# Kernel optimization log

Hardware: AMD Instinct MI355X
Metric: run time of the kernel (lower is better)

## Reference

```python
import jax, jax.numpy as jnp
import numpy as np

H = 1024   # hidden_size == embedding_dim (forced by the 2*hidden concat/view)
A = 256    # attention_hidden_size
V = 50257  # vocab_size
L = 2      # num_layers
T = 512    # decoder length
S = 512    # encoder length


def setup_inputs() -> dict:
    key = jax.random.key(0)
    ks = jax.random.split(key, 24)
    f = lambda i, shape: (0.02 * jax.random.normal(ks[i], shape)).astype(jnp.float32)
    return {
        "decoder_input": jax.random.randint(ks[0], (T,), 0, V),
        "encoder_outputs": jax.random.normal(ks[1], (S, H), dtype=jnp.float32),
        "emb": f(2, (V, H)),
        # attn (context attention over encoder outputs): Linear(2H->A) split into x/ctx parts, v: Linear(A->1)
        "Wa_x": f(3, (A, H)), "Wa_c": f(4, (A, H)), "ba": f(5, (A,)), "va": f(6, (A,)), "vab": f(7, ()),
        # GRU cells (torch GRUCell param layout: [r; z; n] stacked, 3H rows)
        "Wih0": f(8, (3 * H, 2 * H)), "bih0": f(9, (3 * H,)), "Whh0": f(10, (3 * H, H)), "bhh0": f(11, (3 * H,)),
        "Wih1": f(12, (3 * H, H)), "bih1": f(13, (3 * H,)), "Whh1": f(14, (3 * H, H)), "bhh1": f(15, (3 * H,)),
        # per-layer hidden self-attentions (no context)
        "Wh": f(16, (L, A, H)), "bh": f(17, (L, A)), "vh": f(18, (L, A)), "vhb": f(19, (L,)),
        # output head
        "Wf1": f(20, (32, H)), "bf1": f(21, (32,)), "Wf2": f(22, (V, 32)), "bf2": f(23, (V,)),
    }


def _attn(x, Wx, b, v, vb, ctx=None, Wc=None):
    # additive attention: e_t = v . tanh(W_x x_t + W_c c + b); weighted sum over axis 0
    pre = x @ Wx.T + b                      # [T, A]
    if ctx is not None:
        pre = pre + ctx @ Wc.T              # broadcast [A]
    e = jnp.tanh(pre) @ v + vb              # [T]
    return jax.nn.softmax(e) @ x            # [D]


def _gru(x, h, Wih, bih, Whh, bhh):
    gi = Wih @ x + bih
    gh = Whh @ h + bhh
    ir, iz, inn = jnp.split(gi, 3)
    hr, hz, hn = jnp.split(gh, 3)
    r = jax.nn.sigmoid(ir + hr)
    z = jax.nn.sigmoid(iz + hz)
    n = jnp.tanh(inn + r * hn)
    return (1.0 - z) * n + z * h


def reference(decoder_input, encoder_outputs, emb, Wa_x, Wa_c, ba, va, vab,
              Wih0, bih0, Whh0, bhh0, Wih1, bih1, Whh1, bhh1,
              Wh, bh, vh, vhb, Wf1, bf1, Wf2, bf2):
    tok_embs = emb[decoder_input]           # [T, H]

    def step(carry, tok):
        h0, h1 = carry
        a = _attn(encoder_outputs, Wa_x, ba, va, vab, ctx=h0, Wc=Wa_c)  # [H]
        x = jnp.concatenate([a, tok])                                   # [2H]
        nh0 = _gru(x, h0, Wih0, bih0, Whh0, bhh0)
        nh1 = _gru(nh0, h1, Wih1, bih1, Whh1, bhh1)
        # hidden attention i combines new_h_s[i:]
        h0n = _attn(jnp.stack([nh0, nh1]), Wh[0], bh[0], vh[0], vhb[0])
        h1n = _attn(nh1[None, :], Wh[1], bh[1], vh[1], vhb[1])           # softmax over 1 elem == nh1
        fc1 = jax.nn.relu(Wf1 @ h1n + bf1)                               # dropout = eval-mode identity
        out = jax.nn.softmax(Wf2 @ fc1 + bf2)                            # softmax over vocab (dim 0)
        return (h0n, h1n), out

    h0 = jnp.zeros((Whh0.shape[1],), jnp.float32)
    _, outs = jax.lax.scan(step, (h0, h0), tok_embs)
    return outs  # [T, V]
```

## Files before the change

### kernel.cpp

```cpp
#include <hip/hip_runtime.h>
#include <cstdint>
#include <cstddef>

#define T_LEN 512
#define S_LEN 512
#define HID   1024
#define AD    256
#define VOC   50257
#define G3    3072
#define NWG   256
#define NT    512
#define NPART (197*4)

#define WS_GENC   0
#define WS_GITOK  (WS_GENC + G3*S_LEN)
#define WS_EX     (WS_GITOK + T_LEN*G3)
#define WS_H1     (WS_EX + S_LEN*AD)
#define WS_FC1    (WS_H1 + T_LEN*HID)
#define WS_NH0    (WS_FC1 + T_LEN*32)
#define WS_NH1    (WS_NH0 + HID)
#define WS_WB     (WS_NH1 + HID)
#define WS_U0     (WS_WB + S_LEN)
#define WS_U1     (WS_U0 + AD)
#define WS_E0P    (WS_U1 + AD)
#define WS_E1P    (WS_E0P + 256)
#define WS_BARX   (WS_E1P + 256)
#define WS_ROWP   (WS_BARX + 384)
#define WS_INV    (WS_ROWP + T_LEN*NPART)
#define WS_END    (WS_INV + T_LEN)

__device__ inline float wred64(float v) {
  v += __shfl_xor(v, 32, 64); v += __shfl_xor(v, 16, 64); v += __shfl_xor(v, 8, 64);
  v += __shfl_xor(v, 4, 64);  v += __shfl_xor(v, 2, 64);  v += __shfl_xor(v, 1, 64);
  return v;
}

__device__ inline float fast_sigmoid(float x) { return 1.f / (1.f + __expf(-x)); }
__device__ inline float fast_tanh(float x) {
  float e = __expf(2.f * x);
  return 1.f - 2.f / (e + 1.f);
}

__device__ inline float ldw(const float* p) {
  return __uint_as_float(__hip_atomic_load((const unsigned int*)p,
                                           __ATOMIC_RELAXED, __HIP_MEMORY_SCOPE_AGENT));
}
__device__ inline void stw(float* p, float v) {
  __hip_atomic_store((unsigned int*)p, __float_as_uint(v),
                     __ATOMIC_RELAXED, __HIP_MEMORY_SCOPE_AGENT);
}
__device__ inline unsigned ldu(const unsigned* p) {
  return __hip_atomic_load(p, __ATOMIC_RELAXED, __HIP_MEMORY_SCOPE_AGENT);
}
__device__ inline void stu(unsigned* p, unsigned v) {
  __hip_atomic_store(p, v, __ATOMIC_RELAXED, __HIP_MEMORY_SCOPE_AGENT);
}

__device__ inline void gbar(unsigned* slot, unsigned* gen, unsigned b) {
  __syncthreads();
  if (threadIdx.x == 0) stu(slot + blockIdx.x, b);
  if (blockIdx.x == 0) {
    if (threadIdx.x < NWG) {
      while (ldu(slot + threadIdx.x) < b) __builtin_amdgcn_s_sleep(1);
    }
    __syncthreads();
    if (threadIdx.x == 0) stu(gen, b);
  } else {
    if (threadIdx.x == 0) {
      while (ldu(gen) < b) __builtin_amdgcn_s_sleep(1);
    }
    __syncthreads();
  }
}

__device__ inline float qdot4(const float4& a0, const float4& a1, const float4& a2, const float4& a3,
                              const float4& x0, const float4& x1, const float4& x2, const float4& x3) {
  float a = 0.f;
  a = fmaf(a0.x, x0.x, a); a = fmaf(a0.y, x0.y, a); a = fmaf(a0.z, x0.z, a); a = fmaf(a0.w, x0.w, a);
  a = fmaf(a1.x, x1.x, a); a = fmaf(a1.y, x1.y, a); a = fmaf(a1.z, x1.z, a); a = fmaf(a1.w, x1.w, a);
  a = fmaf(a2.x, x2.x, a); a = fmaf(a2.y, x2.y, a); a = fmaf(a2.z, x2.z, a); a = fmaf(a2.w, x2.w, a);
  a = fmaf(a3.x, x3.x, a); a = fmaf(a3.y, x3.y, a); a = fmaf(a3.z, x3.z, a); a = fmaf(a3.w, x3.w, a);
  return a;
}
__device__ inline float qdot2(const float4& a0, const float4& a1,
                              const float4& x0, const float4& x1) {
  float a = 0.f;
  a = fmaf(a0.x, x0.x, a); a = fmaf(a0.y, x0.y, a); a = fmaf(a0.z, x0.z, a); a = fmaf(a0.w, x0.w, a);
  a = fmaf(a1.x, x1.x, a); a = fmaf(a1.y, x1.y, a); a = fmaf(a1.z, x1.z, a); a = fmaf(a1.w, x1.w, a);
  return a;
}

__global__ void k_init(float* ws) {
  const int tid = threadIdx.x;
  for (int i = tid; i < HID; i += 256) { ws[WS_NH0 + i] = 0.f; ws[WS_NH1 + i] = 0.f; }
  if (tid < AD) { ws[WS_U0 + tid] = 0.f; ws[WS_U1 + tid] = 0.f; }
  ws[WS_E0P + tid] = 0.f;
  ws[WS_E1P + tid] = 0.f;
  for (int i = tid; i < 384; i += 256) ((unsigned*)(ws + WS_BARX))[i] = 0u;
}

__global__ __launch_bounds__(256) void k_gemm(
    const float* __restrict__ A, int lda, const int* __restrict__ gidx,
    const float* __restrict__ B, int ldb, int kofs,
    const float* __restrict__ bias, float* __restrict__ C, int ldc,
    int M, int N, int act)
{
  __shared__ float As[64][33];
  __shared__ float Bs[64][33];
  const int bm = blockIdx.y * 64, bn = blockIdx.x * 64;
  const int tx = threadIdx.x & 15, ty = threadIdx.x >> 4;
  float acc[4][4] = {};
  const int lin = threadIdx.x * 8;
  const int lr = lin >> 5;
  const int lc = lin & 31;
  for (int k0 = 0; k0 < 1024; k0 += 32) {
    {
      const int gm = bm + lr;
      float4 v0 = {0,0,0,0}, v1 = {0,0,0,0};
      if (gm < M) {
        const int row = gidx ? gidx[gm] : gm;
        const float* p = A + (size_t)row * lda + k0 + lc;
        v0 = *(const float4*)p; v1 = *(const float4*)(p + 4);
      }
      As[lr][lc+0]=v0.x; As[lr][lc+1]=v0.y; As[lr][lc+2]=v0.z; As[lr][lc+3]=v0.w;
      As[lr][lc+4]=v1.x; As[lr][lc+5]=v1.y; As[lr][lc+6]=v1.z; As[lr][lc+7]=v1.w;
    }
    {
      const int gn = bn + lr;
      float4 v0 = {0,0,0,0}, v1 = {0,0,0,0};
      if (gn < N) {
        const float* p = B + (size_t)gn * ldb + kofs + k0 + lc;
        v0 = *(const float4*)p; v1 = *(const float4*)(p + 4);
      }
      Bs[lr][lc+0]=v0.x; Bs[lr][lc+1]=v0.y; Bs[lr][lc+2]=v0.z; Bs[lr][lc+3]=v0.w;
      Bs[lr][lc+4]=v1.x; Bs[lr][lc+5]=v1.y; Bs[lr][lc+6]=v1.z; Bs[lr][lc+7]=v1.w;
    }
    __syncthreads();
    #pragma unroll
    for (int kk = 0; kk < 32; ++kk) {
      float a0 = As[ty*4+0][kk], a1 = As[ty*4+1][kk], a2 = As[ty*4+2][kk], a3 = As[ty*4+3][kk];
      float b0 = Bs[tx*4+0][kk], b1 = Bs[tx*4+1][kk], b2 = Bs[tx*4+2][kk], b3 = Bs[tx*4+3][kk];
      acc[0][0]=fmaf(a0,b0,acc[0][0]); acc[0][1]=fmaf(a0,b1,acc[0][1]); acc[0][2]=fmaf(a0,b2,acc[0][2]); acc[0][3]=fmaf(a0,b3,acc[0][3]);
      acc[1][0]=fmaf(a1,b0,acc[1][0]); acc[1][1]=fmaf(a1,b1,acc[1][1]); acc[1][2]=fmaf(a1,b2,acc[1][2]); acc[1][3]=fmaf(a1,b3,acc[1][3]);
      acc[2][0]=fmaf(a2,b0,acc[2][0]); acc[2][1]=fmaf(a2,b1,acc[2][1]); acc[2][2]=fmaf(a2,b2,acc[2][2]); acc[2][3]=fmaf(a2,b3,acc[2][3]);
      acc[3][0]=fmaf(a3,b0,acc[3][0]); acc[3][1]=fmaf(a3,b1,acc[3][1]); acc[3][2]=fmaf(a3,b2,acc[3][2]); acc[3][3]=fmaf(a3,b3,acc[3][3]);
    }
    __syncthreads();
  }
  #pragma unroll
  for (int i = 0; i < 4; ++i)
    #pragma unroll
    for (int j = 0; j < 4; ++j) {
      const int m = bm + ty*4 + i, n = bn + tx*4 + j;
      if (m < M && n < N) {
        float v = acc[i][j] + (bias ? bias[n] : 0.f);
        if (act == 1) v = fmaxf(v, 0.f);
        C[(size_t)m * ldc + n] = v;
      }
    }
}

__global__ __launch_bounds__(NT) void k_recur(
    float* __restrict__ ws,
    const float* __restrict__ Whh0, const float* __restrict__ bhh0,
    const float* __restrict__ Wih1, const float* __restrict__ bih1,
    const float* __restrict__ Whh1, const float* __restrict__ bhh1,
    const float* __restrict__ Wh,   const float* __restrict__ bh,
    const float* __restrict__ vh,   const float* __restrict__ vhb,
    const float* __restrict__ va,   const float* __restrict__ vab,
    const float* __restrict__ Wac)
{
  const float* Genc  = ws + WS_GENC;
  const float* gitok = ws + WS_GITOK;
  const float* Ex    = ws + WS_EX;
  float* H1    = ws + WS_H1;
  float* nh0g  = ws + WS_NH0;
  float* nh1g  = ws + WS_NH1;
  float* wbufg = ws + WS_WB;
  float* u0g   = ws + WS_U0;
  float* u1g   = ws + WS_U1;
  float* e0pg  = ws + WS_E0P;
  float* e1pg  = ws + WS_E1P;
  unsigned* slot = (unsigned*)(ws + WS_BARX);
  unsigned* gen  = slot + NWG;

  const int wg = blockIdx.x, tid = threadIdx.x;
  const int lane = tid & 63, wv = tid >> 6;

  __shared__ float xv[HID];
  __shared__ float wl[S_LEN];
  __shared__ float cb[AD];
  __shared__ float sgit[12], sgh0[12], gh1l[12], sb0[12], sbh1[12], sacc[12];
  __shared__ float sred[8], sal[2], ssc[1];

  float4 wreg[28];
  if (wv < 6) {
    #pragma unroll
    for (int r = 0; r < 2; ++r) {
      const int lr = 2 * wv + r;
      const int g = (lr >> 2) * HID + wg * 4 + (lr & 3);
      const float4* p0 = (const float4*)(Whh0 + (size_t)g * HID);
      const float4* p1 = (const float4*)(Wih1 + (size_t)g * HID);
      const float4* p2 = (const float4*)(Whh1 + (size_t)g * HID);
      const float4* pg = (const float4*)(Genc + (size_t)g * S_LEN);
      #pragma unroll
      for (int p = 0; p < 4; ++p) {
        wreg[r*4+p]      = p0[p*64 + lane];
        wreg[8 + r*4+p]  = p1[p*64 + lane];
        wreg[16 + r*4+p] = p2[p*64 + lane];
      }
      #pragma unroll
      for (int p = 0; p < 2; ++p) wreg[24 + r*2+p] = pg[p*64 + lane];
    }
  } else {
    const float* Wrow = (wv == 6) ? (Wh + (size_t)wg * HID) : (Wac + (size_t)wg * HID);
    const float4* p0 = (const float4*)Wrow;
    #pragma unroll
    for (int p = 0; p < 4; ++p) wreg[p] = p0[p*64 + lane];
    const int s = 2 * wg + (wv - 6);
    wreg[4] = ((const float4*)(Ex + (size_t)s * AD))[lane];
    wreg[5] = ((const float4*)va)[lane];
  }

  float i1r = 0.f, i1z = 0.f, i1n = 0.f;
  if (tid < 4) {
    const int j = wg * 4 + tid;
    i1r = bih1[j]; i1z = bih1[HID + j]; i1n = bih1[2 * HID + j];
  }
  if (tid < 12) {
    const int g = (tid >> 2) * HID + wg * 4 + (tid & 3);
    sb0[tid] = bhh0[g];
    const float bb = bhh1[g];
    sbh1[tid] = bb;
    gh1l[tid] = bb;
  }
  const float vhW = vh[wg], bhW = bh[wg];
  const float vabv = vab[0], vhb0 = vhb[0];
  unsigned b = 0;
  __syncthreads();

  const float4* XV4 = (const float4*)xv;
  const float4* WL4 = (const float4*)wl;
  const float4* CB4 = (const float4*)cb;

  #pragma unroll 1
  for (int t = 0; t < T_LEN; ++t) {
    {
      const float a0 = ldw(nh0g + tid), a1 = ldw(nh0g + 512 + tid);
      const float b0 = ldw(nh1g + tid), b1 = ldw(nh1g + 512 + tid);
      float uu0 = 0.f, uu1 = 0.f;
      if (tid < AD) { uu0 = ldw(u0g + tid); uu1 = ldw(u1g + tid); }
      float ep = (tid < 256) ? ldw(e0pg + tid) : ldw(e1pg + tid - 256);
      if (tid < 12)
        sgit[tid] = gitok[(size_t)t * G3 + (tid >> 2) * HID + wg * 4 + (tid & 3)];
      ep = wred64(ep);
      if (lane == 0) sred[wv] = ep;
      __syncthreads();
      if (tid == 0) {
        const float e0 = sred[0] + sred[1] + sred[2] + sred[3] + vhb0;
        const float e1 = sred[4] + sred[5] + sred[6] + sred[7] + vhb0;
        const float ea = __expf(e0), eb = __expf(e1);
        const float s = ea + eb;
        sal[0] = ea / s; sal[1] = eb / s;
      }
      __syncthreads();
      const float al0 = sal[0], al1 = sal[1];
      xv[tid]       = al0 * a0 + al1 * b0;
      xv[tid + 512] = al0 * a1 + al1 * b1;
      if (tid < AD) cb[tid] = al0 * uu0 + al1 * uu1;
      __syncthreads();
      if (wv < 6) {
        const float4 x0 = XV4[lane], x1 = XV4[64+lane], x2 = XV4[128+lane], x3 = XV4[192+lane];
        float accA = qdot4(wreg[0], wreg[1], wreg[2], wreg[3], x0, x1, x2, x3);
        float accB = qdot4(wreg[4], wreg[5], wreg[6], wreg[7], x0, x1, x2, x3);
        accA = wred64(accA); accB = wred64(accB);
        if (lane == 0) {
          sgh0[2*wv]     = accA + sb0[2*wv];
          sgh0[2*wv + 1] = accB + sb0[2*wv + 1];
        }
      } else {
        const float4 e4 = wreg[4], v4 = wreg[5], c4 = CB4[lane];
        const float s0 = fast_tanh(e4.x + c4.x);
        const float s1 = fast_tanh(e4.y + c4.y);
        const float s2 = fast_tanh(e4.z + c4.z);
        const float s3 = fast_tanh(e4.w + c4.w);
        float acc = v4.x*s0 + v4.y*s1 + v4.z*s2 + v4.w*s3;
        acc = wred64(acc);
        if (lane == 0) stw(wbufg + 2*wg + (wv - 6), __expf(acc + vabv));
      }
    }
    gbar(slot, gen, ++b);

    {
      const float wval = ldw(wbufg + tid);
      wl[tid] = wval;
      const float ps = wred64(wval);
      if (lane == 0) sred[wv] = ps;
      __syncthreads();
      if (tid == 0) {
        float s = 0.f;
        #pragma unroll
        for (int i = 0; i < 8; ++i) s += sred[i];
        ssc[0] = 1.f / s;
      }
      if (wv < 6) {
        const float4 w0 = WL4[lane], w1 = WL4[64 + lane];
        float accA = qdot2(wreg[24], wreg[25], w0, w1);
        float accB = qdot2(wreg[26], wreg[27], w0, w1);
        accA = wred64(accA); accB = wred64(accB);
        if (lane == 0) { sacc[2*wv] = accA; sacc[2*wv + 1] = accB; }
      }
      __syncthreads();
      if (tid < 4) {
        const float inv = ssc[0];
        const float d0 = sacc[tid]     * inv + sgit[tid];
        const float d1 = sacc[4 + tid] * inv + sgit[4 + tid];
        const float d2 = sacc[8 + tid] * inv + sgit[8 + tid];
        const float rg = fast_sigmoid(d0 + sgh0[tid]);
        const float zg = fast_sigmoid(d1 + sgh0[4 + tid]);
        const float ng = fast_tanh(d2 + rg * sgh0[8 + tid]);
        const float h0j = xv[wg * 4 + tid];
        stw(nh0g + wg * 4 + tid, (1.f - zg) * ng + zg * h0j);
      }
    }
    gbar(slot, gen, ++b);

    {
      const float x0 = ldw(nh0g + tid), x1 = ldw(nh0g + 512 + tid);
      const float oldn = (tid < 4) ? ldw(nh1g + wg * 4 + tid) : 0.f;
      xv[tid] = x0; xv[tid + 512] = x1;
      __syncthreads();
      const float4 y0 = XV4[lane], y1 = XV4[64+lane], y2 = XV4[128+lane], y3 = XV4[192+lane];
      if (wv < 6) {
        float accA = qdot4(wreg[8],  wreg[9],  wreg[10], wreg[11], y0, y1, y2, y3);
        float accB = qdot4(wreg[12], wreg[13], wreg[14], wreg[15], y0, y1, y2, y3);
        accA = wred64(accA); accB = wred64(accB);
        if (lane == 0) { sacc[2*wv] = accA; sacc[2*wv + 1] = accB; }
      } else {
        float acc = qdot4(wreg[0], wreg[1], wreg[2], wreg[3], y0, y1, y2, y3);
        acc = wred64(acc);
        if (lane == 0) {
          if (wv == 6) stw(e0pg + wg, vhW * fast_tanh(acc + bhW));
          else         stw(u0g + wg, acc);
        }
      }
      __syncthreads();
      if (tid < 4) {
        const float gr = sacc[tid]     + i1r;
        const float gz = sacc[4 + tid] + i1z;
        const float gn = sacc[8 + tid] + i1n;
        const float rg = fast_sigmoid(gr + gh1l[tid]);
        const float zg = fast_sigmoid(gz + gh1l[4 + tid]);
        const float ng = fast_tanh(gn + rg * gh1l[8 + tid]);
        const float nv = (1.f - zg) * ng + zg * oldn;
        stw(nh1g + wg * 4 + tid, nv);
        H1[(size_t)t * HID + wg * 4 + tid] = nv;
      }
    }
    gbar(slot, gen, ++b);

    {
      const float x0 = ldw(nh1g + tid), x1 = ldw(nh1g + 512 + tid);
      xv[tid] = x0; xv[tid + 512] = x1;
      __syncthreads();
      const float4 y0 = XV4[lane], y1 = XV4[64+lane], y2 = XV4[128+lane], y3 = XV4[192+lane];
      if (wv < 6) {
        float accA = qdot4(wreg[16], wreg[17], wreg[18], wreg[19], y0, y1, y2, y3);
        float accB = qdot4(wreg[20], wreg[21], wreg[22], wreg[23], y0, y1, y2, y3);
        accA = wred64(accA); accB = wred64(accB);
        if (lane == 0) {
          gh1l[2*wv]     = accA + sbh1[2*wv];
          gh1l[2*wv + 1] = accB + sbh1[2*wv + 1];
        }
      } else {
        float acc = qdot4(wreg[0], wreg[1], wreg[2], wreg[3], y0, y1, y2, y3);
        acc = wred64(acc);
        if (lane == 0) {
          if (wv == 6) stw(e1pg + wg, vhW * fast_tanh(acc + bhW));
          else         stw(u1g + wg, acc);
        }
      }
    }
    gbar(slot, gen, ++b);
  }
}

__global__ __launch_bounds__(256) void k_head(
    const float* __restrict__ FC1, const float* __restrict__ Wf2,
    const float* __restrict__ bf2, float* __restrict__ out, float* __restrict__ rowp)
{
  __shared__ float fcb[256 * 32];
  const int v = blockIdx.x * 256 + threadIdx.x;
  const bool ok = v < VOC;
  float wf[32];
  float bb = 0.f;
  if (ok) {
    const float4* W4 = (const float4*)(Wf2 + (size_t)v * 32);
    #pragma unroll
    for (int q = 0; q < 8; ++q) ((float4*)wf)[q] = W4[q];
    bb = bf2[v];
  }
  const int wv = threadIdx.x >> 6;
  #pragma unroll 1
  for (int half = 0; half < 2; ++half) {
    __syncthreads();
    for (int i = threadIdx.x; i < 256 * 32 / 4; i += 256)
      ((float4*)fcb)[i] = ((const float4*)(FC1 + half * 256 * 32))[i];
    __syncthreads();
    #pragma unroll 1
    for (int tt = 0; tt < 256; ++tt) {
      const int t = half * 256 + tt;
      const float4* f4 = (const float4*)(fcb + tt * 32);
      float acc = bb;
      #pragma unroll
      for (int q = 0; q < 8; ++q) {
        float4 f = f4[q];
        acc = fmaf(wf[4*q+0], f.x, acc);
        acc = fmaf(wf[4*q+1], f.y, acc);
        acc = fmaf(wf[4*q+2], f.z, acc);
        acc = fmaf(wf[4*q+3], f.w, acc);
      }
      const float w = ok ? __expf(acc) : 0.f;
      if (ok) out[(size_t)t * VOC + v] = w;
      float r = wred64(w);
      if ((threadIdx.x & 63) == 0)
        rowp[(size_t)t * NPART + (size_t)blockIdx.x * 4 + wv] = r;
    }
  }
}

__global__ __launch_bounds__(256) void k_rowsum(const float* __restrict__ rowp, float* __restrict__ inv) {
  const int t = blockIdx.x;
  float acc = 0.f;
  for (int i = threadIdx.x; i < NPART; i += 256) acc += rowp[(size_t)t * NPART + i];
  acc = wred64(acc);
  __shared__ float sr[4];
  if ((threadIdx.x & 63) == 0) sr[threadIdx.x >> 6] = acc;
  __syncthreads();
  if (threadIdx.x == 0) inv[t] = 1.f / (sr[0] + sr[1] + sr[2] + sr[3]);
}

__global__ __launch_bounds__(256) void k_scale(float* __restrict__ out, const float* __restrict__ inv) {
  const int t = blockIdx.y;
  const float s = inv[t];
  const size_t base = (size_t)t * VOC;
  const int v0 = blockIdx.x * 2048 + threadIdx.x;
  #pragma unroll
  for (int k = 0; k < 8; ++k) {
    const int v = v0 + k * 256;
    if (v < VOC) out[base + v] *= s;
  }
}

extern "C" void kernel_launch(void* const* d_in, const int* in_sizes, int n_in,
                              void* d_out, int out_size, void* d_ws, size_t ws_size,
                              hipStream_t stream) {
  const int*   dec  = (const int*)  d_in[0];
  const float* enc  = (const float*)d_in[1];
  const float* emb  = (const float*)d_in[2];
  const float* Wax  = (const float*)d_in[3];
  const float* Wac  = (const float*)d_in[4];
  const float* ba   = (const float*)d_in[5];
  const float* va   = (const float*)d_in[6];
  const float* vab  = (const float*)d_in[7];
  const float* Wih0 = (const float*)d_in[8];
  const float* bih0 = (const float*)d_in[9];
  const float* Whh0 = (const float*)d_in[10];
  const float* bhh0 = (const float*)d_in[11];
  const float* Wih1 = (const float*)d_in[12];
  const float* bih1 = (const float*)d_in[13];
  const float* Whh1 = (const float*)d_in[14];
  const float* bhh1 = (const float*)d_in[15];
  const float* Wh   = (const float*)d_in[16];
  const float* bh   = (const float*)d_in[17];
  const float* vh   = (const float*)d_in[18];
  const float* vhb  = (const float*)d_in[19];
  const float* Wf1  = (const float*)d_in[20];
  const float* bf1  = (const float*)d_in[21];
  const float* Wf2  = (const float*)d_in[22];
  const float* bf2  = (const float*)d_in[23];
  float* out = (float*)d_out;
  float* ws  = (float*)d_ws;

  k_init<<<1, 256, 0, stream>>>(ws);

  k_gemm<<<dim3(8, 48), 256, 0, stream>>>(Wih0, 2048, nullptr, enc, 1024, 0,
                                          nullptr, ws + WS_GENC, 512, G3, S_LEN, 0);
  k_gemm<<<dim3(48, 8), 256, 0, stream>>>(emb, 1024, dec, Wih0, 2048, 1024,
                                          bih0, ws + WS_GITOK, G3, T_LEN, G3, 0);
  k_gemm<<<dim3(4, 8), 256, 0, stream>>>(enc, 1024, nullptr, Wax, 1024, 0,
                                         ba, ws + WS_EX, AD, S_LEN, AD, 0);

  k_recur<<<NWG, NT, 0, stream>>>(ws, Whh0, bhh0, Wih1, bih1, Whh1, bhh1,
                                  Wh, bh, vh, vhb, va, vab, Wac);

  k_gemm<<<dim3(1, 8), 256, 0, stream>>>(ws + WS_H1, 1024, nullptr, Wf1, 1024, 0,
                                         bf1, ws + WS_FC1, 32, T_LEN, 32, 1);

  k_head<<<197, 256, 0, stream>>>(ws + WS_FC1, Wf2, bf2, out, ws + WS_ROWP);
  k_rowsum<<<512, 256, 0, stream>>>(ws + WS_ROWP, ws + WS_INV);
  k_scale<<<dim3(25, 512), 256, 0, stream>>>(out, ws + WS_INV);
}
```

Before: 5.518 ms.

## Replace grid barriers with tagged per-value flags and double-buffered exchange

The persistent recurrent kernel no longer runs four centralized grid barriers per timestep. Each exchanged value is now stored as a 64-bit word that packs the float with a timestep tag, double-buffered by step parity. Consumers spin until the exact values they need carry the expected tag, so workgroups sync point-to-point. A few block-level syncs and a serial thread-0 softmax are also folded into redundant per-thread computation. The change aims to remove barrier latency from the serial critical path, at the cost of many more polling atomic loads and more memory-ordering subtlety.

```diff
diff --git a/kernel.cpp b/kernel.cpp
--- a/kernel.cpp
+++ b/kernel.cpp
@@ -12,65 +12,67 @@
 #define NT    512
 #define NPART (197*4)
 
+typedef unsigned long long u64;
+
 #define WS_GENC   0
 #define WS_GITOK  (WS_GENC + G3*S_LEN)
 #define WS_EX     (WS_GITOK + T_LEN*G3)
 #define WS_H1     (WS_EX + S_LEN*AD)
 #define WS_FC1    (WS_H1 + T_LEN*HID)
-#define WS_NH0    (WS_FC1 + T_LEN*32)
-#define WS_NH1    (WS_NH0 + HID)
-#define WS_WB     (WS_NH1 + HID)
-#define WS_U0     (WS_WB + S_LEN)
-#define WS_U1     (WS_U0 + AD)
-#define WS_E0P    (WS_U1 + AD)
-#define WS_E1P    (WS_E0P + 256)
-#define WS_BARX   (WS_E1P + 256)
-#define WS_ROWP   (WS_BARX + 384)
+#define WS_ROWP   (WS_FC1 + T_LEN*32)
 #define WS_INV    (WS_ROWP + T_LEN*NPART)
-#define WS_END    (WS_INV + T_LEN)
+#define WS_TAGF   (((WS_INV + T_LEN) + 3) & ~3)
+
+#define SP 2
+#define TG_NH0 0
+#define TG_NH1 (TG_NH0 + 2*1024*SP)
+#define TG_W   (TG_NH1 + 2*1024*SP)
+#define TG_U0  (TG_W   + 2*512*SP)
+#define TG_U1  (TG_U0  + 2*256*SP)
+#define TG_E0  (TG_U1  + 2*256*SP)
+#define TG_E1  (TG_E0  + 2*256*SP)
+#define TG_TOT (TG_E1  + 2*256*SP)
 
 __device__ inline float wred64(float v) {
   v += __shfl_xor(v, 32, 64); v += __shfl_xor(v, 16, 64); v += __shfl_xor(v, 8, 64);
   v += __shfl_xor(v, 4, 64);  v += __shfl_xor(v, 2, 64);  v += __shfl_xor(v, 1, 64);
   return v;
 }
-
 __device__ inline float fast_sigmoid(float x) { return 1.f / (1.f + __expf(-x)); }
 __device__ inline float fast_tanh(float x) {
   float e = __expf(2.f * x);
   return 1.f - 2.f / (e + 1.f);
 }
 
-__device__ inline float ldw(const float* p) {
-  return __uint_as_float(__hip_atomic_load((const unsigned int*)p,
-                                           __ATOMIC_RELAXED, __HIP_MEMORY_SCOPE_AGENT));
-}
-__device__ inline void stw(float* p, float v) {
-  __hip_atomic_store((unsigned int*)p, __float_as_uint(v),
+__device__ inline u64 ald(const u64* p) {
+  return __hip_atomic_load(p, __ATOMIC_RELAXED, __HIP_MEMORY_SCOPE_AGENT);
+}
+__device__ inline void stq(u64* p, float v, unsigned tag) {
+  __hip_atomic_store(p, ((u64)tag << 32) | (u64)__float_as_uint(v),
                      __ATOMIC_RELAXED, __HIP_MEMORY_SCOPE_AGENT);
 }
-__device__ inline unsigned ldu(const unsigned* p) {
-  return __hip_atomic_load(p, __ATOMIC_RELAXED, __HIP_MEMORY_SCOPE_AGENT);
-}
-__device__ inline void stu(unsigned* p, unsigned v) {
-  __hip_atomic_store(p, v, __ATOMIC_RELAXED, __HIP_MEMORY_SCOPE_AGENT);
-}
-
-__device__ inline void gbar(unsigned* slot, unsigned* gen, unsigned b) {
-  __syncthreads();
-  if (threadIdx.x == 0) stu(slot + blockIdx.x, b);
-  if (blockIdx.x == 0) {
-    if (threadIdx.x < NWG) {
-      while (ldu(slot + threadIdx.x) < b) __builtin_amdgcn_s_sleep(1);
-    }
-    __syncthreads();
-    if (threadIdx.x == 0) stu(gen, b);
-  } else {
-    if (threadIdx.x == 0) {
-      while (ldu(gen) < b) __builtin_amdgcn_s_sleep(1);
-    }
-    __syncthreads();
-  }
+__device__ inline float poll1(const u64* p, unsigned tag) {
+  u64 x = ald(p);
+  while ((unsigned)(x >> 32) != tag) { __builtin_amdgcn_s_sleep(1); x = ald(p); }
+  return __uint_as_float((unsigned)x);
+}
+__device__ inline void poll2(const u64* p0, const u64* p1, unsigned tag, float& r0, float& r1) {
+  u64 x0 = ald(p0), x1 = ald(p1);
+  while (((unsigned)(x0 >> 32) != tag) | ((unsigned)(x1 >> 32) != tag)) {
+    __builtin_amdgcn_s_sleep(1); x0 = ald(p0); x1 = ald(p1);
+  }
+  r0 = __uint_as_float((unsigned)x0); r1 = __uint_as_float((unsigned)x1);
+}
+__device__ inline void poll4(const u64* p0, const u64* p1, const u64* p2, const u64* p3,
+                             unsigned tag, float& r0, float& r1, float& r2, float& r3) {
+  u64 x0 = ald(p0), x1 = ald(p1), x2 = ald(p2), x3 = ald(p3);
+  while (((unsigned)(x0 >> 32) != tag) | ((unsigned)(x1 >> 32) != tag) |
+         ((unsigned)(x2 >> 32) != tag) | ((unsigned)(x3 >> 32) != tag)) {
+    __builtin_amdgcn_s_sleep(1);
+    x0 = ald(p0); x1 = ald(p1); x2 = ald(p2); x3 = ald(p3);
+  }
+  r0 = __uint_as_float((unsigned)x0); r1 = __uint_as_float((unsigned)x1);
+  r2 = __uint_as_float((unsigned)x2); r3 = __uint_as_float((unsigned)x3);
 }
 
 __device__ inline float qdot4(const float4& a0, const float4& a1, const float4& a2, const float4& a3,
@@ -91,12 +93,9 @@
 }
 
 __global__ void k_init(float* ws) {
-  const int tid = threadIdx.x;
-  for (int i = tid; i < HID; i += 256) { ws[WS_NH0 + i] = 0.f; ws[WS_NH1 + i] = 0.f; }
-  if (tid < AD) { ws[WS_U0 + tid] = 0.f; ws[WS_U1 + tid] = 0.f; }
-  ws[WS_E0P + tid] = 0.f;
-  ws[WS_E1P + tid] = 0.f;
-  for (int i = tid; i < 384; i += 256) ((unsigned*)(ws + WS_BARX))[i] = 0u;
+  u64* TG = (u64*)(ws + WS_TAGF);
+  const int i = blockIdx.x * 256 + threadIdx.x;
+  if (i < TG_TOT) TG[i] = 0ull;
 }
 
 __global__ __launch_bounds__(256) void k_gemm(
@@ -173,16 +172,15 @@
   const float* Genc  = ws + WS_GENC;
   const float* gitok = ws + WS_GITOK;
   const float* Ex    = ws + WS_EX;
-  float* H1    = ws + WS_H1;
-  float* nh0g  = ws + WS_NH0;
-  float* nh1g  = ws + WS_NH1;
-  float* wbufg = ws + WS_WB;
-  float* u0g   = ws + WS_U0;
-  float* u1g   = ws + WS_U1;
-  float* e0pg  = ws + WS_E0P;
-  float* e1pg  = ws + WS_E1P;
-  unsigned* slot = (unsigned*)(ws + WS_BARX);
-  unsigned* gen  = slot + NWG;
+  float* H1 = ws + WS_H1;
+  u64* TG   = (u64*)(ws + WS_TAGF);
+  u64* tNH0 = TG + TG_NH0;
+  u64* tNH1 = TG + TG_NH1;
+  u64* tW   = TG + TG_W;
+  u64* tU0  = TG + TG_U0;
+  u64* tU1  = TG + TG_U1;
+  u64* tE0  = TG + TG_E0;
+  u64* tE1  = TG + TG_E1;
 
   const int wg = blockIdx.x, tid = threadIdx.x;
   const int lane = tid & 63, wv = tid >> 6;
@@ -190,8 +188,8 @@
   __shared__ float xv[HID];
   __shared__ float wl[S_LEN];
   __shared__ float cb[AD];
-  __shared__ float sgit[12], sgh0[12], gh1l[12], sb0[12], sbh1[12], sacc[12];
-  __shared__ float sred[8], sal[2], ssc[1];
+  __shared__ float sgh0[12], gh1l[12], sb0[12], sbh1[12], sacc[12];
+  __shared__ float sred[8];
 
   float4 wreg[28];
   if (wv < 6) {
@@ -236,7 +234,6 @@
   }
   const float vhW = vh[wg], bhW = bh[wg];
   const float vabv = vab[0], vhb0 = vhb[0];
-  unsigned b = 0;
   __syncthreads();
 
   const float4* XV4 = (const float4*)xv;
@@ -245,63 +242,71 @@
 
   #pragma unroll 1
   for (int t = 0; t < T_LEN; ++t) {
+    const int c = t & 1, pc = c ^ 1;
+    const unsigned tg = (unsigned)(t + 1);
+    const unsigned tp = (unsigned)t;
+
     {
-      const float a0 = ldw(nh0g + tid), a1 = ldw(nh0g + 512 + tid);
-      const float b0 = ldw(nh1g + tid), b1 = ldw(nh1g + 512 + tid);
-      float uu0 = 0.f, uu1 = 0.f;
-      if (tid < AD) { uu0 = ldw(u0g + tid); uu1 = ldw(u1g + tid); }
-      float ep = (tid < 256) ? ldw(e0pg + tid) : ldw(e1pg + tid - 256);
-      if (tid < 12)
-        sgit[tid] = gitok[(size_t)t * G3 + (tid >> 2) * HID + wg * 4 + (tid & 3)];
+      float a0, a1, b0, b1;
+      poll4(tNH0 + (size_t)(pc*1024 + tid)*SP, tNH0 + (size_t)(pc*1024 + 512 + tid)*SP,
+            tNH1 + (size_t)(pc*1024 + tid)*SP, tNH1 + (size_t)(pc*1024 + 512 + tid)*SP,
+            tp, a0, a1, b0, b1);
+      float ep, uu0 = 0.f, uu1 = 0.f;
+      if (tid < 256) {
+        ep = poll1(tE0 + (size_t)(pc*256 + tid)*SP, tp);
+        poll2(tU0 + (size_t)(pc*256 + tid)*SP, tU1 + (size_t)(pc*256 + tid)*SP, tp, uu0, uu1);
+      } else {
+        ep = poll1(tE1 + (size_t)(pc*256 + tid - 256)*SP, tp);
+      }
       ep = wred64(ep);
       if (lane == 0) sred[wv] = ep;
       __syncthreads();
-      if (tid == 0) {
-        const float e0 = sred[0] + sred[1] + sred[2] + sred[3] + vhb0;
-        const float e1 = sred[4] + sred[5] + sred[6] + sred[7] + vhb0;
-        const float ea = __expf(e0), eb = __expf(e1);
-        const float s = ea + eb;
-        sal[0] = ea / s; sal[1] = eb / s;
-      }
-      __syncthreads();
-      const float al0 = sal[0], al1 = sal[1];
+      const float e0s = sred[0] + sred[1] + sred[2] + sred[3] + vhb0;
+      const float e1s = sred[4] + sred[5] + sred[6] + sred[7] + vhb0;
+      const float ea = __expf(e0s), eb = __expf(e1s);
+      const float rs = 1.f / (ea + eb);
+      const float al0 = ea * rs, al1 = eb * rs;
       xv[tid]       = al0 * a0 + al1 * b0;
       xv[tid + 512] = al0 * a1 + al1 * b1;
-      if (tid < AD) cb[tid] = al0 * uu0 + al1 * uu1;
-      __syncthreads();
-      if (wv < 6) {
-        const float4 x0 = XV4[lane], x1 = XV4[64+lane], x2 = XV4[128+lane], x3 = XV4[192+lane];
-        float accA = qdot4(wreg[0], wreg[1], wreg[2], wreg[3], x0, x1, x2, x3);
-        float accB = qdot4(wreg[4], wreg[5], wreg[6], wreg[7], x0, x1, x2, x3);
-        accA = wred64(accA); accB = wred64(accB);
-        if (lane == 0) {
-          sgh0[2*wv]     = accA + sb0[2*wv];
-          sgh0[2*wv + 1] = accB + sb0[2*wv + 1];
-        }
-      } else {
-        const float4 e4 = wreg[4], v4 = wreg[5], c4 = CB4[lane];
-        const float s0 = fast_tanh(e4.x + c4.x);
-        const float s1 = fast_tanh(e4.y + c4.y);
-        const float s2 = fast_tanh(e4.z + c4.z);
-        const float s3 = fast_tanh(e4.w + c4.w);
-        float acc = v4.x*s0 + v4.y*s1 + v4.z*s2 + v4.w*s3;
-        acc = wred64(acc);
-        if (lane == 0) stw(wbufg + 2*wg + (wv - 6), __expf(acc + vabv));
-      }
-    }
-    gbar(slot, gen, ++b);
+      if (tid < 256) cb[tid] = al0 * uu0 + al1 * uu1;
+      __syncthreads();
+    }
+    float h0j = 0.f;
+    if (tid < 4) h0j = xv[wg * 4 + tid];
+    if (wv < 6) {
+      const float4 x0 = XV4[lane], x1 = XV4[64+lane], x2 = XV4[128+lane], x3 = XV4[192+lane];
+      float accA = qdot4(wreg[0], wreg[1], wreg[2], wreg[3], x0, x1, x2, x3);
+      float accB = qdot4(wreg[4], wreg[5], wreg[6], wreg[7], x0, x1, x2, x3);
+      accA = wred64(accA); accB = wred64(accB);
+      if (lane == 0) {
+        sgh0[2*wv]     = accA + sb0[2*wv];
+        sgh0[2*wv + 1] = accB + sb0[2*wv + 1];
+      }
+    } else {
+      const float4 e4 = wreg[4], v4 = wreg[5], c4 = CB4[lane];
+      float acc = v4.x * fast_tanh(e4.x + c4.x) + v4.y * fast_tanh(e4.y + c4.y)
+                + v4.z * fast_tanh(e4.z + c4.z) + v4.w * fast_tanh(e4.w + c4.w);
+      acc = wred64(acc);
+      if (lane == 0)
+        stq(tW + (size_t)(c*512 + 2*wg + (wv - 6))*SP, __expf(acc + vabv), tg);
+    }
 
     {
-      const float wval = ldw(wbufg + tid);
+      float g0 = 0.f, g1 = 0.f, g2 = 0.f;
+      if (tid < 4) {
+        const float* gp = gitok + (size_t)t * G3 + wg * 4 + tid;
+        g0 = gp[0]; g1 = gp[HID]; g2 = gp[2 * HID];
+      }
+      const float wval = poll1(tW + (size_t)(c*512 + tid)*SP, tg);
       wl[tid] = wval;
-      const float ps = wred64(wval);
-      if (lane == 0) sred[wv] = ps;
-      __syncthreads();
-      if (tid == 0) {
+      __syncthreads();
+      float inv = 0.f;
+      if (wv == 0) {
         float s = 0.f;
         #pragma unroll
-        for (int i = 0; i < 8; ++i) s += sred[i];
-        ssc[0] = 1.f / s;
+        for (int k = 0; k < 8; ++k) s += wl[lane + 64*k];
+        s = wred64(s);
+        inv = 1.f / s;
       }
       if (wv < 6) {
         const float4 w0 = WL4[lane], w1 = WL4[64 + lane];
@@ -312,22 +317,21 @@
       }
       __syncthreads();
       if (tid < 4) {
-        const float inv = ssc[0];
-        const float d0 = sacc[tid]     * inv + sgit[tid];
-        const float d1 = sacc[4 + tid] * inv + sgit[4 + tid];
-        const float d2 = sacc[8 + tid] * inv + sgit[8 + tid];
+        const float d0 = sacc[tid]     * inv + g0;
+        const float d1 = sacc[4 + tid] * inv + g1;
+        const float d2 = sacc[8 + tid] * inv + g2;
         const float rg = fast_sigmoid(d0 + sgh0[tid]);
         const float zg = fast_sigmoid(d1 + sgh0[4 + tid]);
         const float ng = fast_tanh(d2 + rg * sgh0[8 + tid]);
-        const float h0j = xv[wg * 4 + tid];
-        stw(nh0g + wg * 4 + tid, (1.f - zg) * ng + zg * h0j);
-      }
-    }
-    gbar(slot, gen, ++b);
+        stq(tNH0 + (size_t)(c*1024 + wg*4 + tid)*SP, (1.f - zg) * ng + zg * h0j, tg);
+      }
+    }
 
     {
-      const float x0 = ldw(nh0g + tid), x1 = ldw(nh0g + 512 + tid);
-      const float oldn = (tid < 4) ? ldw(nh1g + wg * 4 + tid) : 0.f;
+      float oldn = 0.f;
+      if (tid < 4) oldn = poll1(tNH1 + (size_t)(pc*1024 + wg*4 + tid)*SP, tp);
+      float x0, x1;
+      poll2(tNH0 + (size_t)(c*1024 + tid)*SP, tNH0 + (size_t)(c*1024 + 512 + tid)*SP, tg, x0, x1);
       xv[tid] = x0; xv[tid + 512] = x1;
       __syncthreads();
       const float4 y0 = XV4[lane], y1 = XV4[64+lane], y2 = XV4[128+lane], y3 = XV4[192+lane];
@@ -340,8 +344,8 @@
         float acc = qdot4(wreg[0], wreg[1], wreg[2], wreg[3], y0, y1, y2, y3);
         acc = wred64(acc);
         if (lane == 0) {
-          if (wv == 6) stw(e0pg + wg, vhW * fast_tanh(acc + bhW));
-          else         stw(u0g + wg, acc);
+          if (wv == 6) stq(tE0 + (size_t)(c*256 + wg)*SP, vhW * fast_tanh(acc + bhW), tg);
+          else         stq(tU0 + (size_t)(c*256 + wg)*SP, acc, tg);
         }
       }
       __syncthreads();
@@ -353,14 +357,14 @@
         const float zg = fast_sigmoid(gz + gh1l[4 + tid]);
         const float ng = fast_tanh(gn + rg * gh1l[8 + tid]);
         const float nv = (1.f - zg) * ng + zg * oldn;
-        stw(nh1g + wg * 4 + tid, nv);
+        stq(tNH1 + (size_t)(c*1024 + wg*4 + tid)*SP, nv, tg);
         H1[(size_t)t * HID + wg * 4 + tid] = nv;
       }
     }
-    gbar(slot, gen, ++b);
 
     {
-      const float x0 = ldw(nh1g + tid), x1 = ldw(nh1g + 512 + tid);
+      float x0, x1;
+      poll2(tNH1 + (size_t)(c*1024 + tid)*SP, tNH1 + (size_t)(c*1024 + 512 + tid)*SP, tg, x0, x1);
       xv[tid] = x0; xv[tid + 512] = x1;
       __syncthreads();
       const float4 y0 = XV4[lane], y1 = XV4[64+lane], y2 = XV4[128+lane], y3 = XV4[192+lane];
@@ -376,12 +380,11 @@
         float acc = qdot4(wreg[0], wreg[1], wreg[2], wreg[3], y0, y1, y2, y3);
         acc = wred64(acc);
         if (lane == 0) {
-          if (wv == 6) stw(e1pg + wg, vhW * fast_tanh(acc + bhW));
-          else         stw(u1g + wg, acc);
+          if (wv == 6) stq(tE1 + (size_t)(c*256 + wg)*SP, vhW * fast_tanh(acc + bhW), tg);
+          else         stq(tU1 + (size_t)(c*256 + wg)*SP, acc, tg);
         }
       }
     }
-    gbar(slot, gen, ++b);
   }
 }
 
@@ -482,7 +485,7 @@
   float* out = (float*)d_out;
   float* ws  = (float*)d_ws;
 
-  k_init<<<1, 256, 0, stream>>>(ws);
+  k_init<<<56, 256, 0, stream>>>(ws);
 
   k_gemm<<<dim3(8, 48), 256, 0, stream>>>(Wih0, 2048, nullptr, enc, 1024, 0,
                                           nullptr, ws + WS_GENC, 512, G3, S_LEN, 0);
```

Result: no change. 5.575 ms (+1.0%).

## Use two-level grid barrier and carry recurrent state in registers across steps

Applied to the files above, without the earlier changes.

Replaces the flat grid barrier, where one workgroup polled all 256 slots, with a two-level barrier. Eight leader workgroups each gather 32 slots, synchronise among themselves, then release per-group generation flags, and arrival stores now use release ordering. The recurrent loop also keeps the previous nh0/nh1 values, the e0p/u0 partials and the old layer-1 hidden value in registers, and prefetches the next step's gitok slice during the last phase. This removes redundant global reloads at the start of each step. The barrier area now overlaps the start of the rowp workspace region, which is only safe if the head kernel runs after the recurrence.

```diff
diff --git a/kernel.cpp b/kernel.cpp
--- a/kernel.cpp
+++ b/kernel.cpp
@@ -25,7 +25,7 @@
 #define WS_E0P    (WS_U1 + AD)
 #define WS_E1P    (WS_E0P + 256)
 #define WS_BARX   (WS_E1P + 256)
-#define WS_ROWP   (WS_BARX + 384)
+#define WS_ROWP   (WS_BARX + 128)
 #define WS_INV    (WS_ROWP + T_LEN*NPART)
 #define WS_END    (WS_INV + T_LEN)
 
@@ -52,42 +52,37 @@
 __device__ inline unsigned ldu(const unsigned* p) {
   return __hip_atomic_load(p, __ATOMIC_RELAXED, __HIP_MEMORY_SCOPE_AGENT);
 }
-__device__ inline void stu(unsigned* p, unsigned v) {
-  __hip_atomic_store(p, v, __ATOMIC_RELAXED, __HIP_MEMORY_SCOPE_AGENT);
-}
-
-__device__ inline void gbar(unsigned* slot, unsigned* gen, unsigned b) {
+__device__ inline void stu_rel(unsigned* p, unsigned v) {
+  __hip_atomic_store(p, v, __ATOMIC_RELEASE, __HIP_MEMORY_SCOPE_AGENT);
+}
+
+__device__ inline void gbar(unsigned* bar, int wg, unsigned b) {
+  unsigned* slots = bar;
+  unsigned* xa    = bar + 256;
+  unsigned* geng  = bar + 384;
+  const int g = wg & 7;
   __syncthreads();
-  if (threadIdx.x == 0) stu(slot + blockIdx.x, b);
-  if (blockIdx.x == 0) {
-    if (threadIdx.x < NWG) {
-      while (ldu(slot + threadIdx.x) < b) __builtin_amdgcn_s_sleep(1);
+  if (threadIdx.x == 0) stu_rel(slots + g * 32 + (wg >> 3), b);
+  if (wg < 8) {
+    if (threadIdx.x < 32) {
+      const unsigned* p = slots + wg * 32 + threadIdx.x;
+      while (ldu(p) < b) __builtin_amdgcn_s_sleep(1);
     }
     __syncthreads();
-    if (threadIdx.x == 0) stu(gen, b);
+    if (threadIdx.x == 0) stu_rel(xa + wg * 16, b);
+    if (threadIdx.x < 8) {
+      const unsigned* p = xa + threadIdx.x * 16;
+      while (ldu(p) < b) __builtin_amdgcn_s_sleep(1);
+    }
+    __syncthreads();
+    if (threadIdx.x == 0) stu_rel(geng + wg * 16, b);
   } else {
     if (threadIdx.x == 0) {
-      while (ldu(gen) < b) __builtin_amdgcn_s_sleep(1);
-    }
-    __syncthreads();
-  }
-}
-
-__device__ inline float qdot4(const float4& a0, const float4& a1, const float4& a2, const float4& a3,
-                              const float4& x0, const float4& x1, const float4& x2, const float4& x3) {
-  float a = 0.f;
-  a = fmaf(a0.x, x0.x, a); a = fmaf(a0.y, x0.y, a); a = fmaf(a0.z, x0.z, a); a = fmaf(a0.w, x0.w, a);
-  a = fmaf(a1.x, x1.x, a); a = fmaf(a1.y, x1.y, a); a = fmaf(a1.z, x1.z, a); a = fmaf(a1.w, x1.w, a);
-  a = fmaf(a2.x, x2.x, a); a = fmaf(a2.y, x2.y, a); a = fmaf(a2.z, x2.z, a); a = fmaf(a2.w, x2.w, a);
-  a = fmaf(a3.x, x3.x, a); a = fmaf(a3.y, x3.y, a); a = fmaf(a3.z, x3.z, a); a = fmaf(a3.w, x3.w, a);
-  return a;
-}
-__device__ inline float qdot2(const float4& a0, const float4& a1,
-                              const float4& x0, const float4& x1) {
-  float a = 0.f;
-  a = fmaf(a0.x, x0.x, a); a = fmaf(a0.y, x0.y, a); a = fmaf(a0.z, x0.z, a); a = fmaf(a0.w, x0.w, a);
-  a = fmaf(a1.x, x1.x, a); a = fmaf(a1.y, x1.y, a); a = fmaf(a1.z, x1.z, a); a = fmaf(a1.w, x1.w, a);
-  return a;
+      const unsigned* p = geng + g * 16;
+      while (ldu(p) < b) __builtin_amdgcn_s_sleep(1);
+    }
+  }
+  __syncthreads();
 }
 
 __global__ void k_init(float* ws) {
@@ -96,7 +91,7 @@
   if (tid < AD) { ws[WS_U0 + tid] = 0.f; ws[WS_U1 + tid] = 0.f; }
   ws[WS_E0P + tid] = 0.f;
   ws[WS_E1P + tid] = 0.f;
-  for (int i = tid; i < 384; i += 256) ((unsigned*)(ws + WS_BARX))[i] = 0u;
+  for (int i = tid; i < 512; i += 256) ((unsigned*)(ws + WS_BARX))[i] = 0u;
 }
 
 __global__ __launch_bounds__(256) void k_gemm(
@@ -160,6 +155,23 @@
     }
 }
 
+__device__ inline float qdot4(const float4& a0, const float4& a1, const float4& a2, const float4& a3,
+                              const float4& x0, const float4& x1, const float4& x2, const float4& x3) {
+  float a = 0.f;
+  a = fmaf(a0.x, x0.x, a); a = fmaf(a0.y, x0.y, a); a = fmaf(a0.z, x0.z, a); a = fmaf(a0.w, x0.w, a);
+  a = fmaf(a1.x, x1.x, a); a = fmaf(a1.y, x1.y, a); a = fmaf(a1.z, x1.z, a); a = fmaf(a1.w, x1.w, a);
+  a = fmaf(a2.x, x2.x, a); a = fmaf(a2.y, x2.y, a); a = fmaf(a2.z, x2.z, a); a = fmaf(a2.w, x2.w, a);
+  a = fmaf(a3.x, x3.x, a); a = fmaf(a3.y, x3.y, a); a = fmaf(a3.z, x3.z, a); a = fmaf(a3.w, x3.w, a);
+  return a;
+}
+__device__ inline float qdot2(const float4& a0, const float4& a1,
+                              const float4& x0, const float4& x1) {
+  float a = 0.f;
+  a = fmaf(a0.x, x0.x, a); a = fmaf(a0.y, x0.y, a); a = fmaf(a0.z, x0.z, a); a = fmaf(a0.w, x0.w, a);
+  a = fmaf(a1.x, x1.x, a); a = fmaf(a1.y, x1.y, a); a = fmaf(a1.z, x1.z, a); a = fmaf(a1.w, x1.w, a);
+  return a;
+}
+
 __global__ __launch_bounds__(NT) void k_recur(
     float* __restrict__ ws,
     const float* __restrict__ Whh0, const float* __restrict__ bhh0,
@@ -181,8 +193,7 @@
   float* u1g   = ws + WS_U1;
   float* e0pg  = ws + WS_E0P;
   float* e1pg  = ws + WS_E1P;
-  unsigned* slot = (unsigned*)(ws + WS_BARX);
-  unsigned* gen  = slot + NWG;
+  unsigned* bar = (unsigned*)(ws + WS_BARX);
 
   const int wg = blockIdx.x, tid = threadIdx.x;
   const int lane = tid & 63, wv = tid >> 6;
@@ -233,10 +244,16 @@
     const float bb = bhh1[g];
     sbh1[tid] = bb;
     gh1l[tid] = bb;
+    sgit[tid] = gitok[(size_t)0 * G3 + g];
   }
   const float vhW = vh[wg], bhW = bh[wg];
   const float vabv = vab[0], vhb0 = vhb[0];
   unsigned b = 0;
+
+  float pa0 = 0.f, pa1 = 0.f;
+  float pb0 = 0.f, pb1 = 0.f;
+  float pep0 = 0.f, puu0 = 0.f;
+  float oldn = 0.f;
   __syncthreads();
 
   const float4* XV4 = (const float4*)xv;
@@ -246,13 +263,9 @@
   #pragma unroll 1
   for (int t = 0; t < T_LEN; ++t) {
     {
-      const float a0 = ldw(nh0g + tid), a1 = ldw(nh0g + 512 + tid);
-      const float b0 = ldw(nh1g + tid), b1 = ldw(nh1g + 512 + tid);
-      float uu0 = 0.f, uu1 = 0.f;
-      if (tid < AD) { uu0 = ldw(u0g + tid); uu1 = ldw(u1g + tid); }
-      float ep = (tid < 256) ? ldw(e0pg + tid) : ldw(e1pg + tid - 256);
-      if (tid < 12)
-        sgit[tid] = gitok[(size_t)t * G3 + (tid >> 2) * HID + wg * 4 + (tid & 3)];
+      float ep, uu1 = 0.f;
+      if (tid < 256) { ep = pep0; uu1 = ldw(u1g + tid); }
+      else           { ep = ldw(e1pg + (tid - 256)); }
       ep = wred64(ep);
       if (lane == 0) sred[wv] = ep;
       __syncthreads();
@@ -265,9 +278,9 @@
       }
       __syncthreads();
       const float al0 = sal[0], al1 = sal[1];
-      xv[tid]       = al0 * a0 + al1 * b0;
-      xv[tid + 512] = al0 * a1 + al1 * b1;
-      if (tid < AD) cb[tid] = al0 * uu0 + al1 * uu1;
+      xv[tid]       = al0 * pa0 + al1 * pb0;
+      xv[tid + 512] = al0 * pa1 + al1 * pb1;
+      if (tid < AD) cb[tid] = al0 * puu0 + al1 * uu1;
       __syncthreads();
       if (wv < 6) {
         const float4 x0 = XV4[lane], x1 = XV4[64+lane], x2 = XV4[128+lane], x3 = XV4[192+lane];
@@ -280,16 +293,13 @@
         }
       } else {
         const float4 e4 = wreg[4], v4 = wreg[5], c4 = CB4[lane];
-        const float s0 = fast_tanh(e4.x + c4.x);
-        const float s1 = fast_tanh(e4.y + c4.y);
-        const float s2 = fast_tanh(e4.z + c4.z);
-        const float s3 = fast_tanh(e4.w + c4.w);
-        float acc = v4.x*s0 + v4.y*s1 + v4.z*s2 + v4.w*s3;
+        float acc = v4.x * fast_tanh(e4.x + c4.x) + v4.y * fast_tanh(e4.y + c4.y)
+                  + v4.z * fast_tanh(e4.z + c4.z) + v4.w * fast_tanh(e4.w + c4.w);
         acc = wred64(acc);
         if (lane == 0) stw(wbufg + 2*wg + (wv - 6), __expf(acc + vabv));
       }
     }
-    gbar(slot, gen, ++b);
+    gbar(bar, wg, ++b);
 
     {
       const float wval = ldw(wbufg + tid);
@@ -323,11 +333,11 @@
         stw(nh0g + wg * 4 + tid, (1.f - zg) * ng + zg * h0j);
       }
     }
-    gbar(slot, gen, ++b);
+    gbar(bar, wg, ++b);
 
     {
       const float x0 = ldw(nh0g + tid), x1 = ldw(nh0g + 512 + tid);
-      const float oldn = (tid < 4) ? ldw(nh1g + wg * 4 + tid) : 0.f;
+      pa0 = x0; pa1 = x1;
       xv[tid] = x0; xv[tid + 512] = x1;
       __syncthreads();
       const float4 y0 = XV4[lane], y1 = XV4[64+lane], y2 = XV4[128+lane], y3 = XV4[192+lane];
@@ -353,16 +363,23 @@
         const float zg = fast_sigmoid(gz + gh1l[4 + tid]);
         const float ng = fast_tanh(gn + rg * gh1l[8 + tid]);
         const float nv = (1.f - zg) * ng + zg * oldn;
+        oldn = nv;
         stw(nh1g + wg * 4 + tid, nv);
         H1[(size_t)t * HID + wg * 4 + tid] = nv;
       }
     }
-    gbar(slot, gen, ++b);
+    gbar(bar, wg, ++b);
 
     {
       const float x0 = ldw(nh1g + tid), x1 = ldw(nh1g + 512 + tid);
+      pb0 = x0; pb1 = x1;
       xv[tid] = x0; xv[tid + 512] = x1;
       __syncthreads();
+      if (tid < 256) { pep0 = ldw(e0pg + tid); puu0 = ldw(u0g + tid); }
+      if (tid < 12) {
+        const int tn = (t + 1 < T_LEN) ? t + 1 : t;
+        sgit[tid] = gitok[(size_t)tn * G3 + (tid >> 2) * HID + wg * 4 + (tid & 3)];
+      }
       const float4 y0 = XV4[lane], y1 = XV4[64+lane], y2 = XV4[128+lane], y3 = XV4[192+lane];
       if (wv < 6) {
         float accA = qdot4(wreg[16], wreg[17], wreg[18], wreg[19], y0, y1, y2, y3);
@@ -381,7 +398,7 @@
         }
       }
     }
-    gbar(slot, gen, ++b);
+    gbar(bar, wg, ++b);
   }
 }
 
```

After: 11.92 ms. +116.1%, slower.
